# Performance work log

Measured on AMD Instinct MI355X. Metric: run time of the kernel, lower is better.

## Reference

```python
import jax, jax.numpy as jnp
import numpy as np
from jax import lax

# Module dims (match init_kwargs / input_specs)
CIN, COUT, K, STRIDE = 8, 16, 3, 2
U = V = 32                      # input spatial size (inshape = (CIN, U, V))
UO = VO = U // STRIDE           # 'same' padding with stride -> 16
IN_DIM = CIN * U * V + 1        # 8193 (homogeneous)
OUT_DIM = COUT * UO * VO + 1    # 4097 (homogeneous)
N = 1024                        # batch (columns of x_affine)


def setup_inputs() -> dict:
    key = jax.random.key(0)
    k1, k2, k3, k4, k5 = jax.random.split(key, 5)
    w = jax.random.normal(k1, (COUT, CIN, K, K), dtype=jnp.float32) * 0.1
    b = jax.random.normal(k2, (COUT,), dtype=jnp.float32) * 0.1
    # Keying matrices (dense stand-ins for the sparse keys); scaled to keep values sane.
    A = jax.random.normal(k3, (OUT_DIM, OUT_DIM), dtype=jnp.float32) / np.sqrt(OUT_DIM)
    Ainv = jax.random.normal(k4, (IN_DIM, IN_DIM), dtype=jnp.float32) / np.sqrt(IN_DIM)
    x_affine = jax.random.normal(k5, (IN_DIM, N), dtype=jnp.float32)
    return {"w": w, "b": b, "A": A, "Ainv": Ainv, "x_affine": x_affine}


def _toeplitz_conv_apply(z, w, b):
    """Apply the affine Toeplitz conv matrix T to z of shape (CIN*U*V+1, N).
    T = [[conv, bias], [0, 1]] so T@z = [conv(z[:-1]) + b*z[-1]; z[-1]]."""
    n = z.shape[1]
    hom = z[-1]                                   # (N,) homogeneous row
    x = z[:-1].T.reshape(n, CIN, U, V)            # (N, CIN, U, V)
    y = lax.conv_general_dilated(
        x, w, window_strides=(STRIDE, STRIDE), padding="SAME",
        dimension_numbers=("NCHW", "OIHW", "NCHW"))  # (N, COUT, UO, VO)
    y = y + b[None, :, None, None] * hom[:, None, None, None]
    yf = y.reshape(n, COUT * UO * VO).T           # (COUT*UO*VO, N)
    return jnp.concatenate([yf, hom[None, :]], axis=0)  # (OUT_DIM, N)


def reference(w, b, A, Ainv, x_affine):
    # What @ x = A @ T @ Ainv @ x  (factored; never materializes What)
    z = Ainv @ x_affine                # (IN_DIM, N)
    t = _toeplitz_conv_apply(z, w, b)  # (OUT_DIM, N)
    return A @ t                       # (OUT_DIM, N)
```

## Files before the change

kernel.cpp:

```cpp
#include <hip/hip_runtime.h>

#define IN_DIM 8193
#define OUT_DIM 4097
#define NB 1024
#define MP1 8320
#define KP1 8256
#define MP2 4224
#define KP2 4160

typedef __attribute__((ext_vector_type(8))) short short8;
typedef __attribute__((ext_vector_type(4))) float f32x4;

__device__ __forceinline__ unsigned short f2bf(float f) {
  unsigned int u = __float_as_uint(f);
  u = (u + 0x7fffu + ((u >> 16) & 1u)) >> 16;
  return (unsigned short)u;
}

__global__ __launch_bounds__(256) void cvt_pad_kernel(
    const float* __restrict__ src, unsigned short* __restrict__ dst,
    int sR, int sC, int dR, int dC) {
  int gid = blockIdx.x * 256 + threadIdx.x;
  int i4 = gid * 4;
  if (i4 >= dR * dC) return;
  int r = i4 / dC;
  int c = i4 - r * dC;
  unsigned short o[4];
#pragma unroll
  for (int j = 0; j < 4; ++j) {
    int cc = c + j;
    float v = (r < sR && cc < sC) ? src[(size_t)r * sC + cc] : 0.f;
    o[j] = f2bf(v);
  }
  unsigned int lo = (unsigned)o[0] | ((unsigned)o[1] << 16);
  unsigned int hi = (unsigned)o[2] | ((unsigned)o[3] << 16);
  *reinterpret_cast<uint2*>(dst + i4) = make_uint2(lo, hi);
}

__global__ __launch_bounds__(256) void transpose_cvt_kernel(
    const float* __restrict__ src, unsigned short* __restrict__ dst,
    int K, int N, int Kp) {
  __shared__ float tl[32][33];
  const int ntk = Kp >> 5;
  int bx = blockIdx.x % ntk;
  int by = blockIdx.x / ntk;
  int k0 = bx * 32, n0 = by * 32;
  int tx = threadIdx.x & 31, ty = threadIdx.x >> 5;
#pragma unroll
  for (int i = 0; i < 4; ++i) {
    int k = k0 + ty + i * 8;
    tl[ty + i * 8][tx] = (k < K) ? src[(size_t)k * N + n0 + tx] : 0.f;
  }
  __syncthreads();
#pragma unroll
  for (int i = 0; i < 4; ++i) {
    int n = n0 + ty + i * 8;
    dst[(size_t)n * Kp + k0 + tx] = f2bf(tl[tx][ty + i * 8]);
  }
}

__global__ __launch_bounds__(256) void gemm_bt(
    const unsigned short* __restrict__ Ab,
    const unsigned short* __restrict__ Bt,
    float* __restrict__ C,
    int Kp, int Mout, int N) {
  __shared__ unsigned short As[128 * 64];
  __shared__ unsigned short Bs[128 * 64];
  const int tid = threadIdx.x;
  const int wid = tid >> 6;
  const int lane = tid & 63;
  const int nbn = N >> 7;
  const int bm = blockIdx.x / nbn;
  const int bn = blockIdx.x - bm * nbn;
  const int m0 = bm << 7, n0 = bn << 7;
  const int wm = (wid >> 1) << 6;
  const int wn = (wid & 1) << 6;

  f32x4 acc[4][4] = {};

  const int nk = Kp >> 6;
  for (int kt = 0; kt < nk; ++kt) {
    const int k0 = kt << 6;
#pragma unroll
    for (int i = 0; i < 4; ++i) {
      const int s = i * 256 + tid;
      const int row = s >> 3;
      const int gl = (s & 7) ^ (row & 7);
      const unsigned short* ga = Ab + (size_t)(m0 + row) * Kp + (k0 + gl * 8);
      const unsigned short* gb = Bt + (size_t)(n0 + row) * Kp + (k0 + gl * 8);
      unsigned short* la = As + (size_t)(i * 256 + wid * 64) * 8;
      unsigned short* lb = Bs + (size_t)(i * 256 + wid * 64) * 8;
      __builtin_amdgcn_global_load_lds(
          (const __attribute__((address_space(1))) void*)ga,
          (__attribute__((address_space(3))) void*)la, 16, 0, 0);
      __builtin_amdgcn_global_load_lds(
          (const __attribute__((address_space(1))) void*)gb,
          (__attribute__((address_space(3))) void*)lb, 16, 0, 0);
    }
    __syncthreads();
#pragma unroll
    for (int kk = 0; kk < 2; ++kk) {
      short8 af[4], bfr[4];
#pragma unroll
      for (int mf = 0; mf < 4; ++mf) {
        const int row = wm + mf * 16 + (lane & 15);
        const int g = (kk * 4 + (lane >> 4)) ^ (row & 7);
        af[mf] = *reinterpret_cast<const short8*>(As + row * 64 + g * 8);
      }
#pragma unroll
      for (int nf = 0; nf < 4; ++nf) {
        const int row = wn + nf * 16 + (lane & 15);
        const int g = (kk * 4 + (lane >> 4)) ^ (row & 7);
        bfr[nf] = *reinterpret_cast<const short8*>(Bs + row * 64 + g * 8);
      }
#pragma unroll
      for (int mf = 0; mf < 4; ++mf)
#pragma unroll
        for (int nf = 0; nf < 4; ++nf)
          asm volatile("v_mfma_f32_16x16x32_bf16 %0, %1, %2, %0"
                       : "+v"(acc[mf][nf])
                       : "v"(af[mf]), "v"(bfr[nf]));
    }
    __syncthreads();
  }
#pragma unroll
  for (int mf = 0; mf < 4; ++mf) {
    const int rbase = m0 + wm + mf * 16 + (lane >> 4) * 4;
#pragma unroll
    for (int nf = 0; nf < 4; ++nf) {
      const int col = n0 + wn + nf * 16 + (lane & 15);
#pragma unroll
      for (int r = 0; r < 4; ++r) {
        const int row = rbase + r;
        if (row < Mout) C[(size_t)row * N + col] = acc[mf][nf][r];
      }
    }
  }
}

__global__ __launch_bounds__(256) void conv_tT_kernel(
    const float* __restrict__ z, const float* __restrict__ w,
    const float* __restrict__ bias, unsigned short* __restrict__ tT) {
  const int gid = blockIdx.x * 256 + threadIdx.x;
  const int n = gid & 1023;
  const int rg = gid >> 10;
  const int r0 = rg << 3;
  const float hom = z[(size_t)8192 * 1024 + n];
  unsigned short o[8];
  if (r0 >= 4096) {
#pragma unroll
    for (int j = 0; j < 8; ++j) o[j] = f2bf((r0 + j == 4096) ? hom : 0.f);
  } else {
    const int co = r0 >> 8;
    const int uo = (r0 >> 4) & 15;
    const int vo0 = r0 & 15;
    float acc[8];
    const float bb = bias[co];
#pragma unroll
    for (int j = 0; j < 8; ++j) acc[j] = bb * hom;
    for (int ci = 0; ci < 8; ++ci) {
#pragma unroll
      for (int kh = 0; kh < 3; ++kh) {
        const int u = uo * 2 + kh;
        if (u >= 32) continue;
        const float* zbase = z + (size_t)(ci * 1024 + u * 32) * 1024 + n;
#pragma unroll
        for (int kw = 0; kw < 3; ++kw) {
          const float wv = w[((co * 8 + ci) * 3 + kh) * 3 + kw];
#pragma unroll
          for (int j = 0; j < 8; ++j) {
            const int v = (vo0 + j) * 2 + kw;
            if (v < 32) acc[j] += wv * zbase[(size_t)v * 1024];
          }
        }
      }
    }
#pragma unroll
    for (int j = 0; j < 8; ++j) o[j] = f2bf(acc[j]);
  }
  uint4 pv;
  pv.x = (unsigned)o[0] | ((unsigned)o[1] << 16);
  pv.y = (unsigned)o[2] | ((unsigned)o[3] << 16);
  pv.z = (unsigned)o[4] | ((unsigned)o[5] << 16);
  pv.w = (unsigned)o[6] | ((unsigned)o[7] << 16);
  *reinterpret_cast<uint4*>(tT + (size_t)n * KP2 + r0) = pv;
}

extern "C" void kernel_launch(void* const* d_in, const int* in_sizes, int n_in,
                              void* d_out, int out_size, void* d_ws, size_t ws_size,
                              hipStream_t stream) {
  const float* w    = (const float*)d_in[0];
  const float* bias = (const float*)d_in[1];
  const float* A    = (const float*)d_in[2];
  const float* Ainv = (const float*)d_in[3];
  const float* x    = (const float*)d_in[4];
  float* out = (float*)d_out;

  char* ws = (char*)d_ws;
  size_t off = 0;
  unsigned short* Ainv_b = (unsigned short*)(ws + off); off += (size_t)MP1 * KP1 * 2;
  unsigned short* xT_b   = (unsigned short*)(ws + off); off += (size_t)NB * KP1 * 2;
  float*          z      = (float*)(ws + off);          off += (size_t)IN_DIM * NB * 4;
  unsigned short* A2_b   = (unsigned short*)(ws + off); off += (size_t)MP2 * KP2 * 2;
  unsigned short* tT_b   = (unsigned short*)(ws + off); off += (size_t)NB * KP2 * 2;
  (void)ws_size; (void)in_sizes; (void)n_in; (void)out_size;

  cvt_pad_kernel<<<(MP1 * KP1 / 4 + 255) / 256, 256, 0, stream>>>(
      Ainv, Ainv_b, IN_DIM, IN_DIM, MP1, KP1);
  transpose_cvt_kernel<<<(KP1 / 32) * (NB / 32), 256, 0, stream>>>(
      x, xT_b, IN_DIM, NB, KP1);
  cvt_pad_kernel<<<(MP2 * KP2 / 4 + 255) / 256, 256, 0, stream>>>(
      A, A2_b, OUT_DIM, OUT_DIM, MP2, KP2);
  gemm_bt<<<(MP1 / 128) * (NB / 128), 256, 0, stream>>>(
      Ainv_b, xT_b, z, KP1, IN_DIM, NB);
  conv_tT_kernel<<<(520 * 1024) / 256, 256, 0, stream>>>(z, w, bias, tT_b);
  gemm_bt<<<(MP2 / 128) * (NB / 128), 256, 0, stream>>>(
      A2_b, tT_b, out, KP2, OUT_DIM, NB);
}
```

Baseline: 518.5 us.

## Replace tiled GEMM with persistent stream-K GEMM using 256x256 tiles and atomics

Replaces the 128x128-tile GEMM with a persistent stream-K kernel. It launches 256 blocks of 512 threads, and each block gets a contiguous range of (tile, k-step) units. Tiles grow to 256x256, loads are double-buffered in LDS through global_load_lds, MFMA runs under raised priority, and partial sums are flushed with atomic adds into zero-initialised outputs. The aim is to balance work across all CUs and increase reuse per loaded byte. It adds zeroing kernels, atomic traffic and nondeterministic summation order, and reuses the Ainv buffer for A to save workspace.

After: 439.8 us. 1.18x faster.

```diff
diff --git a/kernel.cpp b/kernel.cpp
--- a/kernel.cpp
+++ b/kernel.cpp
@@ -3,9 +3,9 @@
 #define IN_DIM 8193
 #define OUT_DIM 4097
 #define NB 1024
-#define MP1 8320
+#define MP1 8448
 #define KP1 8256
-#define MP2 4224
+#define MP2 4352
 #define KP2 4160
 
 typedef __attribute__((ext_vector_type(8))) short short8;
@@ -59,83 +59,148 @@
   }
 }
 
-__global__ __launch_bounds__(256) void gemm_bt(
+__global__ __launch_bounds__(256) void zero_kernel(float4* __restrict__ p, int n) {
+  int i = blockIdx.x * 256 + threadIdx.x;
+  if (i < n) p[i] = make_float4(0.f, 0.f, 0.f, 0.f);
+}
+
+template <int NKT>
+__global__ __launch_bounds__(512) void gemm_sk(
     const unsigned short* __restrict__ Ab,
     const unsigned short* __restrict__ Bt,
     float* __restrict__ C,
-    int Kp, int Mout, int N) {
-  __shared__ unsigned short As[128 * 64];
-  __shared__ unsigned short Bs[128 * 64];
+    int Kp, int Mout, int total_units) {
+  extern __shared__ unsigned short lds[];
   const int tid = threadIdx.x;
   const int wid = tid >> 6;
   const int lane = tid & 63;
-  const int nbn = N >> 7;
-  const int bm = blockIdx.x / nbn;
-  const int bn = blockIdx.x - bm * nbn;
-  const int m0 = bm << 7, n0 = bn << 7;
-  const int wm = (wid >> 1) << 6;
-  const int wn = (wid & 1) << 6;
-
-  f32x4 acc[4][4] = {};
-
-  const int nk = Kp >> 6;
-  for (int kt = 0; kt < nk; ++kt) {
-    const int k0 = kt << 6;
-#pragma unroll
-    for (int i = 0; i < 4; ++i) {
-      const int s = i * 256 + tid;
-      const int row = s >> 3;
-      const int gl = (s & 7) ^ (row & 7);
-      const unsigned short* ga = Ab + (size_t)(m0 + row) * Kp + (k0 + gl * 8);
-      const unsigned short* gb = Bt + (size_t)(n0 + row) * Kp + (k0 + gl * 8);
-      unsigned short* la = As + (size_t)(i * 256 + wid * 64) * 8;
-      unsigned short* lb = Bs + (size_t)(i * 256 + wid * 64) * 8;
-      __builtin_amdgcn_global_load_lds(
-          (const __attribute__((address_space(1))) void*)ga,
-          (__attribute__((address_space(3))) void*)la, 16, 0, 0);
-      __builtin_amdgcn_global_load_lds(
-          (const __attribute__((address_space(1))) void*)gb,
-          (__attribute__((address_space(3))) void*)lb, 16, 0, 0);
+  const int wm = (wid >> 2) << 7;
+  const int wn = (wid & 3) << 6;
+  const int b = blockIdx.x;
+  const int bw = ((b & 7) << 5) | (b >> 3);
+  const int s = (int)(((long long)bw * total_units) >> 8);
+  const int e = (int)(((long long)(bw + 1) * total_units) >> 8);
+
+  const int g0 = ((lane >> 4) ^ (lane & 7)) * 8;
+  const int g1 = ((4 + (lane >> 4)) ^ (lane & 7)) * 8;
+  const int alo = (lane & 15) * 64;
+  const int bhalf = (wn >> 7) << 1;
+  const int ahalf = (wid >> 2) << 1;
+  const int bsub = ((wn & 64) << 6) + alo;
+
+#define STAGE(UNIT, ISA)                                                       \
+  do {                                                                         \
+    const int rq_ = (UNIT);                                                    \
+    const int us_ = rq_ < e - 1 ? rq_ : e - 1;                                 \
+    const int par_ = rq_ & 1;                                                  \
+    const int tau_ = us_ / NKT;                                                \
+    const int kt_ = us_ - tau_ * NKT;                                          \
+    const size_t gr_ = (size_t)((ISA) ? (tau_ >> 2) : (tau_ & 3)) << 8;        \
+    const unsigned short* M_ = (ISA) ? Ab : Bt;                                \
+    _Pragma("unroll")                                                          \
+    for (int h_ = 0; h_ < 2; ++h_) {                                           \
+      _Pragma("unroll")                                                        \
+      for (int L_ = 0; L_ < 2; ++L_) {                                         \
+        const int s_ = L_ * 512 + tid;                                         \
+        const int row_ = s_ >> 3;                                              \
+        const int gl_ = (s_ & 7) ^ (row_ & 7);                                 \
+        const unsigned short* g_ = M_ + (gr_ + (h_ << 7) + row_) * (size_t)Kp  \
+                                      + (kt_ << 6) + gl_ * 8;                  \
+        unsigned short* l_ = lds + (((ISA) ? 0 : 4) + (h_ << 1) + par_) * 8192 \
+                                 + (size_t)(L_ * 512 + wid * 64) * 8;          \
+        __builtin_amdgcn_global_load_lds(                                      \
+            (const __attribute__((address_space(1))) void*)g_,                 \
+            (__attribute__((address_space(3))) void*)l_, 16, 0, 0);            \
+      }                                                                        \
+    }                                                                          \
+  } while (0)
+
+#define MFMA16(BV0, BV1, NF0, NF1)                                             \
+  do {                                                                         \
+    __builtin_amdgcn_s_setprio(1);                                             \
+    _Pragma("unroll")                                                          \
+    for (int mf_ = 0; mf_ < 8; ++mf_) {                                        \
+      asm volatile("v_mfma_f32_16x16x32_bf16 %0, %1, %2, %0"                   \
+                   : "+v"(acc[mf_][NF0]) : "v"(af[mf_]), "v"(BV0));            \
+      asm volatile("v_mfma_f32_16x16x32_bf16 %0, %1, %2, %0"                   \
+                   : "+v"(acc[mf_][NF1]) : "v"(af[mf_]), "v"(BV1));            \
+    }                                                                          \
+    __builtin_amdgcn_s_setprio(0);                                             \
+  } while (0)
+
+#define FLUSH(TAU)                                                             \
+  do {                                                                         \
+    const int bm_ = (TAU) >> 2, bn_ = (TAU) & 3;                               \
+    _Pragma("unroll")                                                          \
+    for (int mf_ = 0; mf_ < 8; ++mf_) {                                        \
+      const int rb_ = (bm_ << 8) + wm + mf_ * 16 + ((lane >> 4) << 2);         \
+      _Pragma("unroll")                                                        \
+      for (int nf_ = 0; nf_ < 4; ++nf_) {                                      \
+        const int col_ = (bn_ << 8) + wn + nf_ * 16 + (lane & 15);             \
+        _Pragma("unroll")                                                      \
+        for (int r_ = 0; r_ < 4; ++r_) {                                       \
+          const int row_ = rb_ + r_;                                           \
+          if (row_ < Mout)                                                     \
+            unsafeAtomicAdd(&C[(size_t)row_ * NB + col_], acc[mf_][nf_][r_]);  \
+        }                                                                      \
+        acc[mf_][nf_] = (f32x4)(0.0f);                                         \
+      }                                                                        \
+    }                                                                          \
+  } while (0)
+
+  f32x4 acc[8][4];
+#pragma unroll
+  for (int i = 0; i < 8; ++i)
+#pragma unroll
+    for (int j = 0; j < 4; ++j) acc[i][j] = (f32x4)(0.0f);
+
+  STAGE(s, 1);
+  STAGE(s, 0);
+  STAGE(s + 1, 1);
+
+  int tau_cur = s / NKT;
+  for (int u = s; u < e; ++u) {
+    const int par = u & 1;
+    const unsigned short* Ab_ = lds + (ahalf + par) * 8192 + alo;
+    const unsigned short* Bb_ = lds + (4 + bhalf + par) * 8192 + bsub;
+    short8 af[8], b0, b1;
+    __builtin_amdgcn_sched_barrier(0);
+    asm volatile("s_waitcnt vmcnt(4)" ::: "memory");
+    __builtin_amdgcn_s_barrier();
+    __builtin_amdgcn_sched_barrier(0);
+    STAGE(u + 1, 0);
+#pragma unroll
+    for (int mf = 0; mf < 8; ++mf)
+      af[mf] = *reinterpret_cast<const short8*>(Ab_ + mf * 1024 + g0);
+    b0 = *reinterpret_cast<const short8*>(Bb_ + 0 * 1024 + g0);
+    b1 = *reinterpret_cast<const short8*>(Bb_ + 1 * 1024 + g0);
+    MFMA16(b0, b1, 0, 1);
+    b0 = *reinterpret_cast<const short8*>(Bb_ + 2 * 1024 + g0);
+    b1 = *reinterpret_cast<const short8*>(Bb_ + 3 * 1024 + g0);
+    MFMA16(b0, b1, 2, 3);
+#pragma unroll
+    for (int mf = 0; mf < 8; ++mf)
+      af[mf] = *reinterpret_cast<const short8*>(Ab_ + mf * 1024 + g1);
+    b0 = *reinterpret_cast<const short8*>(Bb_ + 2 * 1024 + g1);
+    b1 = *reinterpret_cast<const short8*>(Bb_ + 3 * 1024 + g1);
+    MFMA16(b0, b1, 2, 3);
+    __builtin_amdgcn_sched_barrier(0);
+    __builtin_amdgcn_s_barrier();
+    __builtin_amdgcn_sched_barrier(0);
+    STAGE(u + 2, 1);
+    b0 = *reinterpret_cast<const short8*>(Bb_ + 0 * 1024 + g1);
+    b1 = *reinterpret_cast<const short8*>(Bb_ + 1 * 1024 + g1);
+    MFMA16(b0, b1, 0, 1);
+    if (u + 1 >= e) {
+      FLUSH(tau_cur);
+    } else {
+      const int tn = (u + 1) / NKT;
+      if (tn != tau_cur) { FLUSH(tau_cur); tau_cur = tn; }
     }
-    __syncthreads();
-#pragma unroll
-    for (int kk = 0; kk < 2; ++kk) {
-      short8 af[4], bfr[4];
-#pragma unroll
-      for (int mf = 0; mf < 4; ++mf) {
-        const int row = wm + mf * 16 + (lane & 15);
-        const int g = (kk * 4 + (lane >> 4)) ^ (row & 7);
-        af[mf] = *reinterpret_cast<const short8*>(As + row * 64 + g * 8);
-      }
-#pragma unroll
-      for (int nf = 0; nf < 4; ++nf) {
-        const int row = wn + nf * 16 + (lane & 15);
-        const int g = (kk * 4 + (lane >> 4)) ^ (row & 7);
-        bfr[nf] = *reinterpret_cast<const short8*>(Bs + row * 64 + g * 8);
-      }
-#pragma unroll
-      for (int mf = 0; mf < 4; ++mf)
-#pragma unroll
-        for (int nf = 0; nf < 4; ++nf)
-          asm volatile("v_mfma_f32_16x16x32_bf16 %0, %1, %2, %0"
-                       : "+v"(acc[mf][nf])
-                       : "v"(af[mf]), "v"(bfr[nf]));
-    }
-    __syncthreads();
-  }
-#pragma unroll
-  for (int mf = 0; mf < 4; ++mf) {
-    const int rbase = m0 + wm + mf * 16 + (lane >> 4) * 4;
-#pragma unroll
-    for (int nf = 0; nf < 4; ++nf) {
-      const int col = n0 + wn + nf * 16 + (lane & 15);
-#pragma unroll
-      for (int r = 0; r < 4; ++r) {
-        const int row = rbase + r;
-        if (row < Mout) C[(size_t)row * N + col] = acc[mf][nf][r];
-      }
-    }
-  }
+  }
+#undef STAGE
+#undef MFMA16
+#undef FLUSH
 }
 
 __global__ __launch_bounds__(256) void conv_tT_kernel(
@@ -197,23 +262,32 @@
   float* out = (float*)d_out;
 
   char* ws = (char*)d_ws;
-  size_t off = 0;
-  unsigned short* Ainv_b = (unsigned short*)(ws + off); off += (size_t)MP1 * KP1 * 2;
-  unsigned short* xT_b   = (unsigned short*)(ws + off); off += (size_t)NB * KP1 * 2;
-  float*          z      = (float*)(ws + off);          off += (size_t)IN_DIM * NB * 4;
-  unsigned short* A2_b   = (unsigned short*)(ws + off); off += (size_t)MP2 * KP2 * 2;
-  unsigned short* tT_b   = (unsigned short*)(ws + off); off += (size_t)NB * KP2 * 2;
+  unsigned short* Ainv_b = (unsigned short*)ws;
+  unsigned short* xT_b   = (unsigned short*)(ws + (size_t)MP1 * KP1 * 2);
+  float*          z      = (float*)(ws + (size_t)MP1 * KP1 * 2 + (size_t)NB * KP1 * 2);
+  unsigned short* tT_b   = (unsigned short*)(ws + (size_t)MP1 * KP1 * 2 + (size_t)NB * KP1 * 2
+                                             + (size_t)MP1 * NB * 4);
+  unsigned short* A2_b   = Ainv_b;
   (void)ws_size; (void)in_sizes; (void)n_in; (void)out_size;
+
+  hipFuncSetAttribute((const void*)gemm_sk<129>,
+                      hipFuncAttributeMaxDynamicSharedMemorySize, 131072);
+  hipFuncSetAttribute((const void*)gemm_sk<65>,
+                      hipFuncAttributeMaxDynamicSharedMemorySize, 131072);
 
   cvt_pad_kernel<<<(MP1 * KP1 / 4 + 255) / 256, 256, 0, stream>>>(
       Ainv, Ainv_b, IN_DIM, IN_DIM, MP1, KP1);
   transpose_cvt_kernel<<<(KP1 / 32) * (NB / 32), 256, 0, stream>>>(
       x, xT_b, IN_DIM, NB, KP1);
+  zero_kernel<<<(MP1 * NB / 4 + 255) / 256, 256, 0, stream>>>(
+      (float4*)z, MP1 * NB / 4);
+  gemm_sk<129><<<256, 512, 131072, stream>>>(
+      Ainv_b, xT_b, z, KP1, MP1, 33 * 4 * 129);
+  conv_tT_kernel<<<(520 * 1024) / 256, 256, 0, stream>>>(z, w, bias, tT_b);
   cvt_pad_kernel<<<(MP2 * KP2 / 4 + 255) / 256, 256, 0, stream>>>(
       A, A2_b, OUT_DIM, OUT_DIM, MP2, KP2);
-  gemm_bt<<<(MP1 / 128) * (NB / 128), 256, 0, stream>>>(
-      Ainv_b, xT_b, z, KP1, IN_DIM, NB);
-  conv_tT_kernel<<<(520 * 1024) / 256, 256, 0, stream>>>(z, w, bias, tT_b);
-  gemm_bt<<<(MP2 / 128) * (NB / 128), 256, 0, stream>>>(
-      A2_b, tT_b, out, KP2, OUT_DIM, NB);
-}
+  zero_kernel<<<(OUT_DIM * NB / 4 + 255) / 256, 256, 0, stream>>>(
+      (float4*)out, OUT_DIM * NB / 4);
+  gemm_sk<65><<<256, 512, 131072, stream>>>(
+      A2_b, tT_b, out, KP2, OUT_DIM, 17 * 4 * 65);
+}
```
